# Performance work log

Measured on AMD Instinct MI355X. Metric: run time of the kernel, lower is better.

The kernel has to match this reference:

```python
import jax, jax.numpy as jnp
import numpy as np

B, P, D_IN, D_MOD, N_HEADS = 512, 64, 64, 256, 4

def _ln(x, g, b):
    m = x.mean(-1, keepdims=True)
    v = ((x - m) ** 2).mean(-1, keepdims=True)
    return (x - m) / jnp.sqrt(v + 1e-5) * g + b

def _lin(x, w, b):
    return x @ w.T + b

def _mha(q, k, v, in_w, in_b, out_w, out_b, n_heads):
    # Faithful to torch nn.MultiheadAttention(batch_first=False): dim0=seq, dim1=batch.
    S, N, E = q.shape
    dh = E // n_heads
    wq, wk, wv = jnp.split(in_w, 3, axis=0)
    bq, bk, bv = jnp.split(in_b, 3)
    qp = _lin(q, wq, bq).reshape(S, N, n_heads, dh)
    kp = _lin(k, wk, bk).reshape(S, N, n_heads, dh)
    vp = _lin(v, wv, bv).reshape(S, N, n_heads, dh)
    scores = jnp.einsum('snhd,tnhd->nhst', qp, kp) * (1.0 / np.sqrt(dh))
    attn = jax.nn.softmax(scores, axis=-1)
    o = jnp.einsum('nhst,tnhd->snhd', attn, vp).reshape(S, N, E)
    return _lin(o, out_w, out_b)

def _forward(x, emb_w, emb_b, emb_g, emb_beta, post_w, post_b, post_g, post_beta,
             attn_qw, attn_qb, attn_kw, attn_kb, attn_vw, attn_vb,
             attn_inw, attn_inb, attn_outw, attn_outb, attn_g, attn_beta,
             player_w, player_b, player_g, player_beta,
             team_w, team_b, team_g, team_beta,
             pre_w, pre_b, pre_g, pre_beta, lnf_g, lnf_b, pred_w, pred_b):
    # embedding: LinearWithLayerNorm = LayerNorm(Linear(x))
    p = _ln(_lin(x, emb_w, emb_b), emb_g, emb_beta)
    # post_embedding: ResidualLinearWithLayerNorm = LayerNorm(Linear(x)) + x
    p = _ln(_lin(p, post_w, post_b), post_g, post_beta) + p
    for i in range(2):
        res = p
        q = _lin(p, attn_qw[i], attn_qb[i])
        k = _lin(p, attn_kw[i], attn_kb[i])
        v = _lin(p, attn_vw[i], attn_vb[i])
        a = _mha(q, k, v, attn_inw[i], attn_inb[i], attn_outw[i], attn_outb[i], N_HEADS)
        p = _ln(a, attn_g[i], attn_beta[i]) + res
    for i in range(2):
        p = _ln(_lin(p, player_w[i], player_b[i]), player_g[i], player_beta[i]) + p
    # segment reduce: padded-ragged scatter + sum == masked sum over the player axis.
    # NOTE: original code computes BOTH masks as original[:,:,-1]==1 (bug preserved).
    mask = (x[:, :, -1] == 1).astype(p.dtype)  # [B, P]
    home = jnp.einsum('bpd,bp->bd', p, mask)
    away = home
    teams = jnp.concatenate([home, away], axis=1)  # [B, 2*d_mod]
    for i in range(2):
        teams = _ln(_lin(teams, team_w[i], team_b[i]), team_g[i], team_beta[i]) + teams
    o = _ln(_lin(teams, pre_w, pre_b), pre_g, pre_beta)
    o = _ln(o, lnf_g, lnf_b)
    o = _lin(o, pred_w, pred_b)[:, 0]  # squeeze(dim=1)
    return o


def setup_inputs() -> dict:
    key = jax.random.key(0)
    ks = iter(jax.random.split(key, 64))
    def nrm(shape):
        return jax.random.normal(next(ks), shape, jnp.float32) * 0.02
    x = jax.random.normal(next(ks), (B, P, D_IN), jnp.float32)
    flag = jax.random.bernoulli(next(ks), 0.5, (B, P)).astype(jnp.float32)
    x = x.at[:, :, -1].set(flag)  # binary home-team indicator channel
    d, d2 = D_MOD, 2 * D_MOD
    return dict(
        x=x,
        emb_w=nrm((d, D_IN)), emb_b=jnp.zeros(d), emb_g=jnp.ones(d), emb_beta=jnp.zeros(d),
        post_w=nrm((d, d)), post_b=jnp.zeros(d), post_g=jnp.ones(d), post_beta=jnp.zeros(d),
        attn_qw=nrm((2, d, d)), attn_qb=jnp.zeros((2, d)),
        attn_kw=nrm((2, d, d)), attn_kb=jnp.zeros((2, d)),
        attn_vw=nrm((2, d, d)), attn_vb=jnp.zeros((2, d)),
        attn_inw=nrm((2, 3 * d, d)), attn_inb=jnp.zeros((2, 3 * d)),
        attn_outw=nrm((2, d, d)), attn_outb=jnp.zeros((2, d)),
        attn_g=jnp.ones((2, d)), attn_beta=jnp.zeros((2, d)),
        player_w=nrm((2, d, d)), player_b=jnp.zeros((2, d)),
        player_g=jnp.ones((2, d)), player_beta=jnp.zeros((2, d)),
        team_w=nrm((2, d2, d2)), team_b=jnp.zeros((2, d2)),
        team_g=jnp.ones((2, d2)), team_beta=jnp.zeros((2, d2)),
        pre_w=nrm((d, d2)), pre_b=jnp.zeros(d), pre_g=jnp.ones(d), pre_beta=jnp.zeros(d),
        lnf_g=jnp.ones(d), lnf_b=jnp.zeros(d),
        pred_w=nrm((1, d)), pred_b=jnp.zeros(1),
    )


def reference(x, emb_w, emb_b, emb_g, emb_beta, post_w, post_b, post_g, post_beta,
              attn_qw, attn_qb, attn_kw, attn_kb, attn_vw, attn_vb,
              attn_inw, attn_inb, attn_outw, attn_outb, attn_g, attn_beta,
              player_w, player_b, player_g, player_beta,
              team_w, team_b, team_g, team_beta,
              pre_w, pre_b, pre_g, pre_beta, lnf_g, lnf_b, pred_w, pred_b):
    return _forward(x, emb_w, emb_b, emb_g, emb_beta, post_w, post_b, post_g, post_beta,
                    attn_qw, attn_qb, attn_kw, attn_kb, attn_vw, attn_vb,
                    attn_inw, attn_inb, attn_outw, attn_outb, attn_g, attn_beta,
                    player_w, player_b, player_g, player_beta,
                    team_w, team_b, team_g, team_beta,
                    pre_w, pre_b, pre_g, pre_beta, lnf_g, lnf_b, pred_w, pred_b)
```

## Files before the change

### kernel.cpp

```cpp
#include <hip/hip_runtime.h>
#include <math.h>


typedef __bf16 bf16x8 __attribute__((ext_vector_type(8)));
typedef __bf16 bf16x4 __attribute__((ext_vector_type(4)));
typedef __bf16 bf16x2 __attribute__((ext_vector_type(2)));
typedef float  f32x4  __attribute__((ext_vector_type(4)));
typedef unsigned short u16;
typedef unsigned short u16x8 __attribute__((ext_vector_type(8)));

__device__ __forceinline__ u16 f2b(float f) {
    unsigned int u = __builtin_bit_cast(unsigned int, f);
    return (u16)((u + 0x7fffu + ((u >> 16) & 1u)) >> 16);
}
__device__ __forceinline__ float b2f(u16 u) {
    unsigned int v = ((unsigned int)u) << 16;
    return __builtin_bit_cast(float, v);
}
__device__ __forceinline__ bf16x8 ld2x64(const u16* p) {
    bf16x4 lo = *(const bf16x4*)p;
    bf16x4 hi = *(const bf16x4*)(p + 4);
    return __builtin_shufflevector(lo, hi, 0, 1, 2, 3, 4, 5, 6, 7);
}
__device__ __forceinline__ bf16x8 ld4x32(const u16* p) {
    bf16x2 a = *(const bf16x2*)p,     b = *(const bf16x2*)(p + 2);
    bf16x2 c = *(const bf16x2*)(p + 4), d = *(const bf16x2*)(p + 6);
    bf16x4 lo = __builtin_shufflevector(a, b, 0, 1, 2, 3);
    bf16x4 hi = __builtin_shufflevector(c, d, 0, 1, 2, 3);
    return __builtin_shufflevector(lo, hi, 0, 1, 2, 3, 4, 5, 6, 7);
}
__device__ __forceinline__ void split8(const float* __restrict__ s,
                                       bf16x8& hi, bf16x8& lo) {
    u16x8 h, l;
    #pragma unroll
    for (int j = 0; j < 8; ++j) {
        float v  = s[j];
        u16  hb  = f2b(v);
        h[j] = hb;
        l[j] = f2b(v - b2f(hb));
    }
    hi = __builtin_bit_cast(bf16x8, h);
    lo = __builtin_bit_cast(bf16x8, l);
}

template<int IN, bool LN, bool RES, bool AF32, int OMODE, bool TEAM>
__device__ __forceinline__
void gemm_body(const void* __restrict__ Xa, const void* __restrict__ Xb, int ldX,
               const u16* __restrict__ Whi, const u16* __restrict__ Wlo,
               const float* __restrict__ bias,
               const float* __restrict__ g, const float* __restrict__ beta,
               const u16* __restrict__ resh, const u16* __restrict__ resl,
               int ldRes, void* __restrict__ Y0, void* __restrict__ Y1, int ldY,
               const float* __restrict__ xmask, float* __restrict__ teams,
               u16* __restrict__ Wb)
{
    constexpr int KT = IN / 32;
    const int tid = threadIdx.x;
    const int wv = tid >> 6, lane = tid & 63;
    const int quad = lane >> 4, l16 = lane & 15;
    const long arow = (long)blockIdx.x * 64 + wv * 16 + l16;

    const u16* sbase[8];
    int sdst[8];
    #pragma unroll
    for (int i = 0; i < 8; ++i) {
        int cid = tid + i * 256;
        int plane = cid >> 10, nt = (cid >> 6) & 15, slot = cid & 63;
        int q = slot >> 4, c = slot & 15;
        sbase[i] = (plane ? Wlo : Whi) + (long)(nt * 16 + c) * IN + q * 8;
        sdst[i]  = (plane * 16 + nt) * 512 + slot * 8;
    }
    u16x8 wreg[8];
    auto issueW = [&](int kt) {
        #pragma unroll
        for (int i = 0; i < 8; ++i) wreg[i] = *(const u16x8*)(sbase[i] + kt * 32);
    };
    auto commitW = [&](int buf) {
        #pragma unroll
        for (int i = 0; i < 8; ++i)
            *(u16x8*)&Wb[buf * 16384 + sdst[i]] = wreg[i];
    };

    bf16x8 ah[3], al[3];
    auto loadA = [&](int kt) {
        int s = kt % 3;
        long aofs = arow * (long)ldX + kt * 32 + quad * 8;
        if constexpr (AF32) {
            float av[8];
            *(f32x4*)&av[0] = *(const f32x4*)&((const float*)Xa)[aofs];
            *(f32x4*)&av[4] = *(const f32x4*)&((const float*)Xa)[aofs + 4];
            split8(av, ah[s], al[s]);
        } else {
            ah[s] = *(const bf16x8*)&((const u16*)Xa)[aofs];
            al[s] = *(const bf16x8*)&((const u16*)Xb)[aofs];
        }
    };

    f32x4 acc[16];
    #pragma unroll
    for (int nt = 0; nt < 16; ++nt) acc[nt] = f32x4{0.f, 0.f, 0.f, 0.f};

    issueW(0);
    commitW(0);
    if (KT > 1) issueW(1);
    loadA(0);
    if (KT > 1) loadA(1);
    __syncthreads();

    #pragma unroll
    for (int kt = 0; kt < KT; ++kt) {
        if (kt + 2 < KT) loadA(kt + 2);
        const u16* wb = Wb + (kt & 1) * 16384;
        const int s = kt % 3;
        #pragma unroll
        for (int nt = 0; nt < 16; ++nt) {
            bf16x8 bhi = *(const bf16x8*)&wb[nt * 512 + lane * 8];
            bf16x8 blo = *(const bf16x8*)&wb[(16 + nt) * 512 + lane * 8];
            acc[nt] = __builtin_amdgcn_mfma_f32_16x16x32_bf16(al[s], bhi, acc[nt], 0, 0, 0);
            acc[nt] = __builtin_amdgcn_mfma_f32_16x16x32_bf16(ah[s], blo, acc[nt], 0, 0, 0);
            acc[nt] = __builtin_amdgcn_mfma_f32_16x16x32_bf16(ah[s], bhi, acc[nt], 0, 0, 0);
        }
        if (kt + 1 < KT) {
            commitW((kt + 1) & 1);
            if (kt + 2 < KT) issueW(kt + 2);
            __syncthreads();
        }
    }

    #pragma unroll
    for (int nt = 0; nt < 16; ++nt) {
        float bc = bias[nt * 16 + l16];
        #pragma unroll
        for (int r = 0; r < 4; ++r) acc[nt][r] += bc;
    }

    float mean[4], rstd[4];
    if constexpr (LN) {
        float s1[4] = {0, 0, 0, 0}, s2[4] = {0, 0, 0, 0};
        #pragma unroll
        for (int nt = 0; nt < 16; ++nt)
            #pragma unroll
            for (int r = 0; r < 4; ++r) {
                s1[r] += acc[nt][r];
                s2[r] += acc[nt][r] * acc[nt][r];
            }
        #pragma unroll
        for (int off = 1; off < 16; off <<= 1)
            #pragma unroll
            for (int r = 0; r < 4; ++r) {
                s1[r] += __shfl_xor(s1[r], off, 64);
                s2[r] += __shfl_xor(s2[r], off, 64);
            }
        #pragma unroll
        for (int r = 0; r < 4; ++r) {
            mean[r] = s1[r] * (1.0f / 256.f);
            float var = s2[r] * (1.0f / 256.f) - mean[r] * mean[r];
            rstd[r] = rsqrtf(var + 1e-5f);
        }
    }

    if constexpr (TEAM) {
        float m[4];
        #pragma unroll
        for (int r = 0; r < 4; ++r) {
            long row = (long)blockIdx.x * 64 + wv * 16 + quad * 4 + r;
            m[r] = (xmask[row * 64 + 63] == 1.0f) ? 1.0f : 0.0f;
        }
        float ts[16];
        #pragma unroll
        for (int nt = 0; nt < 16; ++nt) {
            int col = nt * 16 + l16;
            float gc = g[col], bc2 = beta[col];
            ts[nt] = 0.f;
            #pragma unroll
            for (int r = 0; r < 4; ++r) {
                long row = (long)blockIdx.x * 64 + wv * 16 + quad * 4 + r;
                float v = (acc[nt][r] - mean[r]) * rstd[r] * gc + bc2;
                v += b2f(resh[row * ldRes + col]) + b2f(resl[row * ldRes + col]);
                ts[nt] += m[r] * v;
            }
        }
        #pragma unroll
        for (int nt = 0; nt < 16; ++nt) {
            ts[nt] += __shfl_xor(ts[nt], 16, 64);
            ts[nt] += __shfl_xor(ts[nt], 32, 64);
        }
        __syncthreads();
        float* tsum = (float*)Wb;
        if (quad == 0) {
            #pragma unroll
            for (int nt = 0; nt < 16; ++nt)
                tsum[wv * 256 + nt * 16 + l16] = ts[nt];
        }
        __syncthreads();
        if (tid < 256) {
            float tot = tsum[tid] + tsum[256 + tid]
                      + tsum[512 + tid] + tsum[768 + tid];
            teams[(long)blockIdx.x * 512 + tid]       = tot;
            teams[(long)blockIdx.x * 512 + 256 + tid] = tot;
        }
        return;
    }

    #pragma unroll
    for (int nt = 0; nt < 16; ++nt) {
        int col = nt * 16 + l16;
        float gc = 1.f, bc2 = 0.f;
        if constexpr (LN) { gc = g[col]; bc2 = beta[col]; }
        #pragma unroll
        for (int r = 0; r < 4; ++r) {
            long row = (long)blockIdx.x * 64 + wv * 16 + quad * 4 + r;
            float v = acc[nt][r];
            if constexpr (LN) v = (v - mean[r]) * rstd[r] * gc + bc2;
            if constexpr (RES)
                v += b2f(resh[row * ldRes + col]) + b2f(resl[row * ldRes + col]);
            long yofs = row * ldY + col;
            if constexpr (OMODE == 0) {
                ((float*)Y0)[yofs] = v;
            } else if constexpr (OMODE == 1) {
                u16 hb = f2b(v);
                ((u16*)Y0)[yofs] = hb;
                ((u16*)Y1)[yofs] = f2b(v - b2f(hb));
            } else if constexpr (OMODE == 2) {
                ((u16*)Y0)[yofs] = f2b(v);
            } else {
                long idx = ((long)((row & 63) * 4 + (col >> 6)) * 512
                            + (row >> 6)) * 64 + (col & 63);
                ((u16*)Y0)[idx] = f2b(v);
            }
        }
    }
}

template<int IN, bool LN, bool RES, bool AF32, int OMODE, bool TEAM>
__global__ __launch_bounds__(256)
void gemm_kernel(const void* __restrict__ Xa, const void* __restrict__ Xb, int ldX,
                 const u16* __restrict__ Whi, const u16* __restrict__ Wlo,
                 const float* __restrict__ bias,
                 const float* __restrict__ g, const float* __restrict__ beta,
                 const u16* __restrict__ resh, const u16* __restrict__ resl,
                 int ldRes, void* __restrict__ Y0, void* __restrict__ Y1, int ldY,
                 const float* __restrict__ xmask, float* __restrict__ teams)
{
    __shared__ u16 Wb[32768];
    gemm_body<IN, LN, RES, AF32, OMODE, TEAM>(Xa, Xb, ldX, Whi, Wlo, bias, g,
                                              beta, resh, resl, ldRes, Y0, Y1,
                                              ldY, xmask, teams, Wb);
}

__global__ __launch_bounds__(256)
void qkv_proj(const u16* __restrict__ ph, const u16* __restrict__ pl,
              const u16* __restrict__ cwL, const float* __restrict__ cb,
              u16* __restrict__ qb, u16* __restrict__ kb, u16* __restrict__ vh)
{
    __shared__ u16 Wb[32768];
    int wsel = blockIdx.y;
    const u16* whi = cwL + (long)wsel * 65536;
    const u16* wlo = cwL + 393216 + (long)wsel * 65536;
    u16* Y = (wsel == 0) ? qb : (wsel == 1) ? kb : vh;
    gemm_body<256, false, false, false, 3, false>(
        ph, pl, 256, whi, wlo, cb + wsel * 256, nullptr, nullptr,
        nullptr, nullptr, 0, Y, nullptr, 256, nullptr, nullptr, Wb);
}

__global__ __launch_bounds__(256)
void combine_kernel(const float* __restrict__ inw, const float* __restrict__ inb,
                    const float* __restrict__ qw, const float* __restrict__ kw,
                    const float* __restrict__ vw, const float* __restrict__ qb,
                    const float* __restrict__ kb, const float* __restrict__ vb,
                    u16* __restrict__ cw, float* __restrict__ cb)
{
    int idx = blockIdx.y, L = idx / 3, wsel = idx % 3;
    const float* Wa = inw + (long)L * 768 * 256 + wsel * 65536;
    const float* ba = inb + L * 768 + wsel * 256;
    const float* Wf = (wsel == 0 ? qw : wsel == 1 ? kw : vw) + (long)L * 65536;
    const float* bf = (wsel == 0 ? qb : wsel == 1 ? kb : vb) + L * 256;

    int o = blockIdx.x, j = threadIdx.x;
    float s = 0.f;
    for (int mm = 0; mm < 256; ++mm)
        s += Wa[o * 256 + mm] * Wf[mm * 256 + j];
    u16 hb = f2b(s);
    cw[(long)idx * 65536 + o * 256 + j] = hb;
    cw[393216 + (long)idx * 65536 + o * 256 + j] = f2b(s - b2f(hb));

    __shared__ float red[256];
    red[j] = Wa[o * 256 + j] * bf[j];
    __syncthreads();
    for (int st = 128; st > 0; st >>= 1) {
        if (j < st) red[j] += red[j + st];
        __syncthreads();
    }
    if (j == 0) cb[idx * 256 + o] = red[0] + ba[o];
}

__global__ __launch_bounds__(256)
void cast_split_multi(const float* s0, u16* d0, int n0,
                      const float* s1, u16* d1, int n1,
                      const float* s2, u16* d2, int n2,
                      const float* s3, u16* d3, int n3,
                      const float* s4, u16* d4, int n4,
                      const float* s5, u16* d5, int n5)
{
    const float* s; u16* d; int n;
    switch (blockIdx.y) {
        case 0: s = s0; d = d0; n = n0; break;
        case 1: s = s1; d = d1; n = n1; break;
        case 2: s = s2; d = d2; n = n2; break;
        case 3: s = s3; d = d3; n = n3; break;
        case 4: s = s4; d = d4; n = n4; break;
        default: s = s5; d = d5; n = n5; break;
    }
    int i = (blockIdx.x * 256 + threadIdx.x) * 4;
    if (i >= n) return;
    float4 v = *(const float4*)&s[i];
    ushort4 h, l;
    h.x = f2b(v.x); l.x = f2b(v.x - b2f(h.x));
    h.y = f2b(v.y); l.y = f2b(v.y - b2f(h.y));
    h.z = f2b(v.z); l.z = f2b(v.z - b2f(h.z));
    h.w = f2b(v.w); l.w = f2b(v.w - b2f(h.w));
    *(ushort4*)&d[i] = h;
    *(ushort4*)&d[n + i] = l;
}

#define VTS 66
#define PS  68
#define EXP2SCALE 0.18033688089184986f

__global__ __launch_bounds__(256)
void attn_kernel(const u16* __restrict__ qbuf, const u16* __restrict__ kbuf,
                 const u16* __restrict__ vh,
                 u16* __restrict__ ofh, u16* __restrict__ ofl)
{
    const int n = blockIdx.x, h = blockIdx.y, sq = blockIdx.z;
    const int tid = threadIdx.x;
    const int wv = tid >> 6, lane = tid & 63;
    const int quad = lane >> 4, l16 = lane & 15;
    const long nhb = (long)(n * 4 + h) * 32768;

    __shared__ u16 Vth[64 * VTS];
    __shared__ u16 Pbh[4][32 * PS];

    bf16x8 qf[2][2];
    #pragma unroll
    for (int rt = 0; rt < 2; ++rt)
        #pragma unroll
        for (int kc = 0; kc < 2; ++kc) {
            long s = sq * 128 + wv * 32 + rt * 16 + l16;
            qf[rt][kc] = *(const bf16x8*)&qbuf[nhb + s * 64 + kc * 32 + quad * 8];
        }

    f32x4 o[2][4];
    #pragma unroll
    for (int rt = 0; rt < 2; ++rt)
        #pragma unroll
        for (int dt = 0; dt < 4; ++dt) o[rt][dt] = f32x4{0.f, 0.f, 0.f, 0.f};
    float l_run[2][4] = {{0.f, 0.f, 0.f, 0.f}, {0.f, 0.f, 0.f, 0.f}};

    for (int tb = 0; tb < 8; ++tb) {
        __syncthreads();
        for (int i = tid; i < 512; i += 256) {
            int t = i >> 3, c = i & 7;
            u16x8 hvv = *(const u16x8*)&vh[nhb + (long)(tb * 64 + t) * 64 + c * 8];
            #pragma unroll
            for (int j = 0; j < 8; ++j)
                Vth[(c * 8 + j) * VTS + t] = hvv[j];
        }
        __syncthreads();

        f32x4 sA[2][4];
        #pragma unroll
        for (int rt = 0; rt < 2; ++rt)
            #pragma unroll
            for (int tt = 0; tt < 4; ++tt) sA[rt][tt] = f32x4{0.f, 0.f, 0.f, 0.f};
        #pragma unroll
        for (int kc = 0; kc < 2; ++kc)
            #pragma unroll
            for (int tt = 0; tt < 4; ++tt) {
                bf16x8 kf = *(const bf16x8*)
                    &kbuf[nhb + (long)(tb * 64 + tt * 16 + l16) * 64
                          + kc * 32 + quad * 8];
                sA[0][tt] = __builtin_amdgcn_mfma_f32_16x16x32_bf16(
                    qf[0][kc], kf, sA[0][tt], 0, 0, 0);
                sA[1][tt] = __builtin_amdgcn_mfma_f32_16x16x32_bf16(
                    qf[1][kc], kf, sA[1][tt], 0, 0, 0);
            }

        #pragma unroll
        for (int rt = 0; rt < 2; ++rt)
            #pragma unroll
            for (int r = 0; r < 4; ++r) {
                float p0 = exp2f(sA[rt][0][r] * EXP2SCALE);
                float p1 = exp2f(sA[rt][1][r] * EXP2SCALE);
                float p2 = exp2f(sA[rt][2][r] * EXP2SCALE);
                float p3 = exp2f(sA[rt][3][r] * EXP2SCALE);
                int prow = (rt * 16 + quad * 4 + r) * PS + l16;
                Pbh[wv][prow +  0] = f2b(p0);
                Pbh[wv][prow + 16] = f2b(p1);
                Pbh[wv][prow + 32] = f2b(p2);
                Pbh[wv][prow + 48] = f2b(p3);
                l_run[rt][r] += (p0 + p1) + (p2 + p3);
            }

        #pragma unroll
        for (int kc = 0; kc < 2; ++kc) {
            bf16x8 pfh[2];
            #pragma unroll
            for (int rt = 0; rt < 2; ++rt)
                pfh[rt] = ld2x64(&Pbh[wv][(rt * 16 + l16) * PS
                                          + kc * 32 + quad * 8]);
            #pragma unroll
            for (int dt = 0; dt < 4; ++dt) {
                bf16x8 vfh = ld4x32(&Vth[(dt * 16 + l16) * VTS
                                         + kc * 32 + quad * 8]);
                o[0][dt] = __builtin_amdgcn_mfma_f32_16x16x32_bf16(
                    pfh[0], vfh, o[0][dt], 0, 0, 0);
                o[1][dt] = __builtin_amdgcn_mfma_f32_16x16x32_bf16(
                    pfh[1], vfh, o[1][dt], 0, 0, 0);
            }
        }
    }

    #pragma unroll
    for (int off = 1; off < 16; off <<= 1)
        #pragma unroll
        for (int rt = 0; rt < 2; ++rt)
            #pragma unroll
            for (int r = 0; r < 4; ++r)
                l_run[rt][r] += __shfl_xor(l_run[rt][r], off, 64);

    #pragma unroll
    for (int rt = 0; rt < 2; ++rt)
        #pragma unroll
        for (int r = 0; r < 4; ++r) {
            float inv = 1.0f / l_run[rt][r];
            long s = sq * 128 + wv * 32 + rt * 16 + quad * 4 + r;
            #pragma unroll
            for (int dt = 0; dt < 4; ++dt) {
                long idx = (s * 64 + n) * 256 + h * 64 + dt * 16 + l16;
                float val = o[rt][dt][r] * inv;
                u16 hb = f2b(val);
                ofh[idx] = hb;
                ofl[idx] = f2b(val - b2f(hb));
            }
        }
}

template<int IN, int OUT, bool RES>
__global__ __launch_bounds__(256)
void tail_gemm(const float* __restrict__ X,
               const u16* __restrict__ Whi, const u16* __restrict__ Wlo,
               const float* __restrict__ bias,
               const float* __restrict__ g, const float* __restrict__ beta,
               const float* __restrict__ res, float* __restrict__ Y)
{
    constexpr int NTW = OUT / 64;
    constexpr int KT  = IN / 32;
    const int tid = threadIdx.x;
    const int wv = tid >> 6, lane = tid & 63;
    const int quad = lane >> 4, l16 = lane & 15;
    const int row0 = blockIdx.x * 16;
    const int colbase = wv * (OUT / 4);

    f32x4 acc[NTW];
    #pragma unroll
    for (int nt = 0; nt < NTW; ++nt) acc[nt] = f32x4{0.f, 0.f, 0.f, 0.f};

    #pragma unroll
    for (int kt = 0; kt < KT; ++kt) {
        float av[8];
        long aofs = (long)(row0 + l16) * IN + kt * 32 + quad * 8;
        *(f32x4*)&av[0] = *(const f32x4*)&X[aofs];
        *(f32x4*)&av[4] = *(const f32x4*)&X[aofs + 4];
        bf16x8 ah, al;
        split8(av, ah, al);
        #pragma unroll
        for (int nt = 0; nt < NTW; ++nt) {
            long wofs = (long)(colbase + nt * 16 + l16) * IN + kt * 32 + quad * 8;
            bf16x8 bhi = *(const bf16x8*)&Whi[wofs];
            bf16x8 blo = *(const bf16x8*)&Wlo[wofs];
            acc[nt] = __builtin_amdgcn_mfma_f32_16x16x32_bf16(al, bhi, acc[nt], 0, 0, 0);
            acc[nt] = __builtin_amdgcn_mfma_f32_16x16x32_bf16(ah, blo, acc[nt], 0, 0, 0);
            acc[nt] = __builtin_amdgcn_mfma_f32_16x16x32_bf16(ah, bhi, acc[nt], 0, 0, 0);
        }
    }

    #pragma unroll
    for (int nt = 0; nt < NTW; ++nt) {
        float bc = bias[colbase + nt * 16 + l16];
        #pragma unroll
        for (int r = 0; r < 4; ++r) acc[nt][r] += bc;
    }

    float s1[4] = {0, 0, 0, 0}, s2[4] = {0, 0, 0, 0};
    #pragma unroll
    for (int nt = 0; nt < NTW; ++nt)
        #pragma unroll
        for (int r = 0; r < 4; ++r) {
            s1[r] += acc[nt][r];
            s2[r] += acc[nt][r] * acc[nt][r];
        }
    #pragma unroll
    for (int off = 1; off < 16; off <<= 1)
        #pragma unroll
        for (int r = 0; r < 4; ++r) {
            s1[r] += __shfl_xor(s1[r], off, 64);
            s2[r] += __shfl_xor(s2[r], off, 64);
        }
    __shared__ float r1[64], r2[64];
    if (l16 == 0) {
        #pragma unroll
        for (int r = 0; r < 4; ++r) {
            r1[wv * 16 + quad * 4 + r] = s1[r];
            r2[wv * 16 + quad * 4 + r] = s2[r];
        }
    }
    __syncthreads();
    float mean[4], rstd[4];
    #pragma unroll
    for (int r = 0; r < 4; ++r) {
        int rr = quad * 4 + r;
        float t1 = r1[rr] + r1[16 + rr] + r1[32 + rr] + r1[48 + rr];
        float t2 = r2[rr] + r2[16 + rr] + r2[32 + rr] + r2[48 + rr];
        mean[r] = t1 * (1.0f / OUT);
        float var = t2 * (1.0f / OUT) - mean[r] * mean[r];
        rstd[r] = rsqrtf(var + 1e-5f);
    }
    #pragma unroll
    for (int nt = 0; nt < NTW; ++nt) {
        int col = colbase + nt * 16 + l16;
        float gc = g[col], bc2 = beta[col];
        #pragma unroll
        for (int r = 0; r < 4; ++r) {
            int row = row0 + quad * 4 + r;
            float v = (acc[nt][r] - mean[r]) * rstd[r] * gc + bc2;
            if constexpr (RES) v += res[(long)row * OUT + col];
            Y[(long)row * OUT + col] = v;
        }
    }
}

__global__ __launch_bounds__(256)
void tail_pred(const float* __restrict__ X,
               const u16* __restrict__ Whi, const u16* __restrict__ Wlo,
               const float* __restrict__ bias,
               const float* __restrict__ g, const float* __restrict__ beta,
               const float* __restrict__ lnf_g, const float* __restrict__ lnf_b,
               const float* __restrict__ pw, const float* __restrict__ pb,
               float* __restrict__ out)
{
    constexpr int IN = 512, OUT = 256, NTW = 4, KT = 16;
    const int tid = threadIdx.x;
    const int wv = tid >> 6, lane = tid & 63;
    const int quad = lane >> 4, l16 = lane & 15;
    const int row0 = blockIdx.x * 16;
    const int colbase = wv * 64;

    f32x4 acc[NTW];
    #pragma unroll
    for (int nt = 0; nt < NTW; ++nt) acc[nt] = f32x4{0.f, 0.f, 0.f, 0.f};

    #pragma unroll
    for (int kt = 0; kt < KT; ++kt) {
        float av[8];
        long aofs = (long)(row0 + l16) * IN + kt * 32 + quad * 8;
        *(f32x4*)&av[0] = *(const f32x4*)&X[aofs];
        *(f32x4*)&av[4] = *(const f32x4*)&X[aofs + 4];
        bf16x8 ah, al;
        split8(av, ah, al);
        #pragma unroll
        for (int nt = 0; nt < NTW; ++nt) {
            long wofs = (long)(colbase + nt * 16 + l16) * IN + kt * 32 + quad * 8;
            bf16x8 bhi = *(const bf16x8*)&Whi[wofs];
            bf16x8 blo = *(const bf16x8*)&Wlo[wofs];
            acc[nt] = __builtin_amdgcn_mfma_f32_16x16x32_bf16(al, bhi, acc[nt], 0, 0, 0);
            acc[nt] = __builtin_amdgcn_mfma_f32_16x16x32_bf16(ah, blo, acc[nt], 0, 0, 0);
            acc[nt] = __builtin_amdgcn_mfma_f32_16x16x32_bf16(ah, bhi, acc[nt], 0, 0, 0);
        }
    }
    #pragma unroll
    for (int nt = 0; nt < NTW; ++nt) {
        float bc = bias[colbase + nt * 16 + l16];
        #pragma unroll
        for (int r = 0; r < 4; ++r) acc[nt][r] += bc;
    }

    __shared__ float r1[64], r2[64];
    float s1[4] = {0, 0, 0, 0}, s2[4] = {0, 0, 0, 0};
    #pragma unroll
    for (int nt = 0; nt < NTW; ++nt)
        #pragma unroll
        for (int r = 0; r < 4; ++r) {
            s1[r] += acc[nt][r];
            s2[r] += acc[nt][r] * acc[nt][r];
        }
    #pragma unroll
    for (int off = 1; off < 16; off <<= 1)
        #pragma unroll
        for (int r = 0; r < 4; ++r) {
            s1[r] += __shfl_xor(s1[r], off, 64);
            s2[r] += __shfl_xor(s2[r], off, 64);
        }
    if (l16 == 0)
        #pragma unroll
        for (int r = 0; r < 4; ++r) {
            r1[wv * 16 + quad * 4 + r] = s1[r];
            r2[wv * 16 + quad * 4 + r] = s2[r];
        }
    __syncthreads();
    float vv[NTW][4];
    #pragma unroll
    for (int r = 0; r < 4; ++r) {
        int rr = quad * 4 + r;
        float t1 = r1[rr] + r1[16 + rr] + r1[32 + rr] + r1[48 + rr];
        float t2 = r2[rr] + r2[16 + rr] + r2[32 + rr] + r2[48 + rr];
        float mean = t1 * (1.0f / OUT);
        float rstd = rsqrtf(t2 * (1.0f / OUT) - mean * mean + 1e-5f);
        #pragma unroll
        for (int nt = 0; nt < NTW; ++nt) {
            int col = colbase + nt * 16 + l16;
            vv[nt][r] = (acc[nt][r] - mean) * rstd * g[col] + beta[col];
        }
    }
    float u1[4] = {0, 0, 0, 0}, u2[4] = {0, 0, 0, 0};
    #pragma unroll
    for (int nt = 0; nt < NTW; ++nt)
        #pragma unroll
        for (int r = 0; r < 4; ++r) {
            u1[r] += vv[nt][r];
            u2[r] += vv[nt][r] * vv[nt][r];
        }
    #pragma unroll
    for (int off = 1; off < 16; off <<= 1)
        #pragma unroll
        for (int r = 0; r < 4; ++r) {
            u1[r] += __shfl_xor(u1[r], off, 64);
            u2[r] += __shfl_xor(u2[r], off, 64);
        }
    __syncthreads();
    if (l16 == 0)
        #pragma unroll
        for (int r = 0; r < 4; ++r) {
            r1[wv * 16 + quad * 4 + r] = u1[r];
            r2[wv * 16 + quad * 4 + r] = u2[r];
        }
    __syncthreads();
    float pd[4];
    #pragma unroll
    for (int r = 0; r < 4; ++r) {
        int rr = quad * 4 + r;
        float t1 = r1[rr] + r1[16 + rr] + r1[32 + rr] + r1[48 + rr];
        float t2 = r2[rr] + r2[16 + rr] + r2[32 + rr] + r2[48 + rr];
        float mean = t1 * (1.0f / OUT);
        float rstd = rsqrtf(t2 * (1.0f / OUT) - mean * mean + 1e-5f);
        pd[r] = 0.f;
        #pragma unroll
        for (int nt = 0; nt < NTW; ++nt) {
            int col = colbase + nt * 16 + l16;
            float v2 = (vv[nt][r] - mean) * rstd * lnf_g[col] + lnf_b[col];
            pd[r] += v2 * pw[col];
        }
    }
    #pragma unroll
    for (int off = 1; off < 16; off <<= 1)
        #pragma unroll
        for (int r = 0; r < 4; ++r)
            pd[r] += __shfl_xor(pd[r], off, 64);
    __syncthreads();
    if (l16 == 0)
        #pragma unroll
        for (int r = 0; r < 4; ++r)
            r1[wv * 16 + quad * 4 + r] = pd[r];
    __syncthreads();
    if (wv == 0 && l16 == 0) {
        #pragma unroll
        for (int r = 0; r < 4; ++r) {
            int rr = quad * 4 + r;
            out[row0 + rr] = r1[rr] + r1[16 + rr] + r1[32 + rr] + r1[48 + rr]
                           + pb[0];
        }
    }
}

extern "C" void kernel_launch(void* const* d_in, const int* in_sizes, int n_in,
                              void* d_out, int out_size, void* d_ws, size_t ws_size,
                              hipStream_t stream)
{
    const float* x         = (const float*)d_in[0];
    const float* emb_w     = (const float*)d_in[1];
    const float* emb_b     = (const float*)d_in[2];
    const float* emb_g     = (const float*)d_in[3];
    const float* emb_beta  = (const float*)d_in[4];
    const float* post_w    = (const float*)d_in[5];
    const float* post_b    = (const float*)d_in[6];
    const float* post_g    = (const float*)d_in[7];
    const float* post_beta = (const float*)d_in[8];
    const float* attn_qw   = (const float*)d_in[9];
    const float* attn_qb   = (const float*)d_in[10];
    const float* attn_kw   = (const float*)d_in[11];
    const float* attn_kb   = (const float*)d_in[12];
    const float* attn_vw   = (const float*)d_in[13];
    const float* attn_vb   = (const float*)d_in[14];
    const float* attn_inw  = (const float*)d_in[15];
    const float* attn_inb  = (const float*)d_in[16];
    const float* attn_outw = (const float*)d_in[17];
    const float* attn_outb = (const float*)d_in[18];
    const float* attn_g    = (const float*)d_in[19];
    const float* attn_beta = (const float*)d_in[20];
    const float* player_w  = (const float*)d_in[21];
    const float* player_b  = (const float*)d_in[22];
    const float* player_g  = (const float*)d_in[23];
    const float* player_bt = (const float*)d_in[24];
    const float* team_w    = (const float*)d_in[25];
    const float* team_b    = (const float*)d_in[26];
    const float* team_g    = (const float*)d_in[27];
    const float* team_beta = (const float*)d_in[28];
    const float* pre_w     = (const float*)d_in[29];
    const float* pre_b     = (const float*)d_in[30];
    const float* pre_g     = (const float*)d_in[31];
    const float* pre_beta  = (const float*)d_in[32];
    const float* lnf_g     = (const float*)d_in[33];
    const float* lnf_b     = (const float*)d_in[34];
    const float* pred_w    = (const float*)d_in[35];
    const float* pred_b    = (const float*)d_in[36];

    char* base = (char*)d_ws;
    const size_t NR = (size_t)32768 * 256;
    u16* ph  = (u16*)base;  base += NR * 2;
    u16* pl  = (u16*)base;  base += NR * 2;
    u16* ofh = (u16*)base;  base += NR * 2;
    u16* ofl = (u16*)base;  base += NR * 2;
    u16* vh  = (u16*)base;  base += NR * 2;
    u16* qb  = (u16*)base;  base += NR * 2;
    u16* kb  = (u16*)base;  base += NR * 2;
    float* teams0 = (float*)base; base += (size_t)512 * 512 * 4;
    float* teams1 = (float*)base; base += (size_t)512 * 512 * 4;
    u16* emb_wp    = (u16*)base;  base += (size_t)2 * 16384 * 2;
    u16* post_wp   = (u16*)base;  base += (size_t)2 * 65536 * 2;
    u16* outw_p    = (u16*)base;  base += (size_t)2 * 131072 * 2;
    u16* player_wp = (u16*)base;  base += (size_t)2 * 131072 * 2;
    u16* team_wp   = (u16*)base;  base += (size_t)2 * 524288 * 2;
    u16* pre_wp    = (u16*)base;  base += (size_t)2 * 131072 * 2;
    u16* cwb       = (u16*)base;  base += (size_t)2 * 393216 * 2;
    float* cbf     = (float*)base; base += (size_t)1536 * 4;

    cast_split_multi<<<dim3(512, 6), 256, 0, stream>>>(
        emb_w, emb_wp, 16384,
        post_w, post_wp, 65536,
        attn_outw, outw_p, 131072,
        player_w, player_wp, 131072,
        team_w, team_wp, 524288,
        pre_w, pre_wp, 131072);

    combine_kernel<<<dim3(256, 6), 256, 0, stream>>>(
        attn_inw, attn_inb, attn_qw, attn_kw, attn_vw,
        attn_qb, attn_kb, attn_vb, cwb, cbf);

    gemm_kernel<64, true, false, true, 1, false><<<512, 256, 0, stream>>>(
        x, nullptr, 64, emb_wp, emb_wp + 16384, emb_b, emb_g, emb_beta,
        nullptr, nullptr, 0, ph, pl, 256, nullptr, nullptr);
    gemm_kernel<256, true, true, false, 1, false><<<512, 256, 0, stream>>>(
        ph, pl, 256, post_wp, post_wp + 65536, post_b, post_g, post_beta,
        ph, pl, 256, ph, pl, 256, nullptr, nullptr);

    for (int L = 0; L < 2; ++L) {
        qkv_proj<<<dim3(512, 3), 256, 0, stream>>>(
            ph, pl, cwb + (size_t)L * 3 * 65536, cbf + L * 768, qb, kb, vh);
        attn_kernel<<<dim3(64, 4, 4), 256, 0, stream>>>(qb, kb, vh, ofh, ofl);
        gemm_kernel<256, true, true, false, 1, false><<<512, 256, 0, stream>>>(
            ofh, ofl, 256, outw_p + (size_t)L * 65536,
            outw_p + 131072 + (size_t)L * 65536, attn_outb + L * 256,
            attn_g + L * 256, attn_beta + L * 256, ph, pl, 256, ph, pl, 256,
            nullptr, nullptr);
    }

    gemm_kernel<256, true, true, false, 1, false><<<512, 256, 0, stream>>>(
        ph, pl, 256, player_wp, player_wp + 131072, player_b,
        player_g, player_bt, ph, pl, 256, ph, pl, 256, nullptr, nullptr);
    gemm_kernel<256, true, true, false, 1, true><<<512, 256, 0, stream>>>(
        ph, pl, 256, player_wp + 65536, player_wp + 131072 + 65536,
        player_b + 256, player_g + 256, player_bt + 256, ph, pl, 256,
        nullptr, nullptr, 256, x, teams0);

    tail_gemm<512, 512, true><<<32, 256, 0, stream>>>(
        teams0, team_wp, team_wp + 524288, team_b,
        team_g, team_beta, teams0, teams1);
    tail_gemm<512, 512, true><<<32, 256, 0, stream>>>(
        teams1, team_wp + 262144, team_wp + 524288 + 262144, team_b + 512,
        team_g + 512, team_beta + 512, teams1, teams0);

    tail_pred<<<32, 256, 0, stream>>>(
        teams0, pre_wp, pre_wp + 131072, pre_b, pre_g, pre_beta,
        lnf_g, lnf_b, pred_w, pred_b, (float*)d_out);
}
```

Baseline: 745.4 us.

## Double-buffer V tile and prefetch K/V into registers in attention kernel

Replaces the two-barrier synchronous V load per key block with a double-buffered LDS tile: V for block tb+2 is prefetched into registers and committed to the alternate buffer while block tb is computed. K fragments for the next block are also prefetched into registers after the QK MFMAs, so global latency overlaps the softmax and PV work. The loop is fully unrolled, there is one barrier per iteration, and the launch bound now requests 4 blocks per CU. This raises register and LDS use, which could cost occupancy or cause spills. It only speeds up the attention part of the larger forward pass.

```diff
diff --git a/kernel.cpp b/kernel.cpp
--- a/kernel.cpp
+++ b/kernel.cpp
@@ -327,7 +327,7 @@
 #define PS  68
 #define EXP2SCALE 0.18033688089184986f
 
-__global__ __launch_bounds__(256)
+__global__ __launch_bounds__(256, 4)
 void attn_kernel(const u16* __restrict__ qbuf, const u16* __restrict__ kbuf,
                  const u16* __restrict__ vh,
                  u16* __restrict__ ofh, u16* __restrict__ ofl)
@@ -338,7 +338,7 @@
     const int quad = lane >> 4, l16 = lane & 15;
     const long nhb = (long)(n * 4 + h) * 32768;
 
-    __shared__ u16 Vth[64 * VTS];
+    __shared__ u16 Vth[2][64 * VTS];
     __shared__ u16 Pbh[4][32 * PS];
 
     bf16x8 qf[2][2];
@@ -350,6 +350,34 @@
             qf[rt][kc] = *(const bf16x8*)&qbuf[nhb + s * 64 + kc * 32 + quad * 8];
         }
 
+    const int vt = tid >> 3, vc = tid & 7;
+    const int vt2 = (tid + 256) >> 3, vc2 = (tid + 256) & 7;
+
+    u16x8 vreg[2];
+    auto loadV = [&](int tb) {
+        vreg[0] = *(const u16x8*)&vh[nhb + (long)(tb * 64 + vt) * 64 + vc * 8];
+        vreg[1] = *(const u16x8*)&vh[nhb + (long)(tb * 64 + vt2) * 64 + vc2 * 8];
+    };
+    auto commitV = [&](int buf) {
+        #pragma unroll
+        for (int j = 0; j < 8; ++j)
+            Vth[buf][(vc * 8 + j) * VTS + vt] = vreg[0][j];
+        #pragma unroll
+        for (int j = 0; j < 8; ++j)
+            Vth[buf][(vc2 * 8 + j) * VTS + vt2] = vreg[1][j];
+    };
+
+    bf16x8 kreg[2][4];
+    auto loadK = [&](int tb) {
+        #pragma unroll
+        for (int kc = 0; kc < 2; ++kc)
+            #pragma unroll
+            for (int tt = 0; tt < 4; ++tt)
+                kreg[kc][tt] = *(const bf16x8*)
+                    &kbuf[nhb + (long)(tb * 64 + tt * 16 + l16) * 64
+                          + kc * 32 + quad * 8];
+    };
+
     f32x4 o[2][4];
     #pragma unroll
     for (int rt = 0; rt < 2; ++rt)
@@ -357,16 +385,15 @@
         for (int dt = 0; dt < 4; ++dt) o[rt][dt] = f32x4{0.f, 0.f, 0.f, 0.f};
     float l_run[2][4] = {{0.f, 0.f, 0.f, 0.f}, {0.f, 0.f, 0.f, 0.f}};
 
+    loadV(0);
+    loadK(0);
+    commitV(0);
+    loadV(1);
+    __syncthreads();
+
+    #pragma unroll
     for (int tb = 0; tb < 8; ++tb) {
-        __syncthreads();
-        for (int i = tid; i < 512; i += 256) {
-            int t = i >> 3, c = i & 7;
-            u16x8 hvv = *(const u16x8*)&vh[nhb + (long)(tb * 64 + t) * 64 + c * 8];
-            #pragma unroll
-            for (int j = 0; j < 8; ++j)
-                Vth[(c * 8 + j) * VTS + t] = hvv[j];
-        }
-        __syncthreads();
+        if (tb + 1 < 8) commitV((tb + 1) & 1);
 
         f32x4 sA[2][4];
         #pragma unroll
@@ -377,14 +404,14 @@
         for (int kc = 0; kc < 2; ++kc)
             #pragma unroll
             for (int tt = 0; tt < 4; ++tt) {
-                bf16x8 kf = *(const bf16x8*)
-                    &kbuf[nhb + (long)(tb * 64 + tt * 16 + l16) * 64
-                          + kc * 32 + quad * 8];
                 sA[0][tt] = __builtin_amdgcn_mfma_f32_16x16x32_bf16(
-                    qf[0][kc], kf, sA[0][tt], 0, 0, 0);
+                    qf[0][kc], kreg[kc][tt], sA[0][tt], 0, 0, 0);
                 sA[1][tt] = __builtin_amdgcn_mfma_f32_16x16x32_bf16(
-                    qf[1][kc], kf, sA[1][tt], 0, 0, 0);
+                    qf[1][kc], kreg[kc][tt], sA[1][tt], 0, 0, 0);
             }
+
+        if (tb + 1 < 8) loadK(tb + 1);
+        if (tb + 2 < 8) loadV(tb + 2);
 
         #pragma unroll
         for (int rt = 0; rt < 2; ++rt)
@@ -411,14 +438,16 @@
                                           + kc * 32 + quad * 8]);
             #pragma unroll
             for (int dt = 0; dt < 4; ++dt) {
-                bf16x8 vfh = ld4x32(&Vth[(dt * 16 + l16) * VTS
-                                         + kc * 32 + quad * 8]);
+                bf16x8 vfh = ld4x32(&Vth[tb & 1][(dt * 16 + l16) * VTS
+                                                 + kc * 32 + quad * 8]);
                 o[0][dt] = __builtin_amdgcn_mfma_f32_16x16x32_bf16(
                     pfh[0], vfh, o[0][dt], 0, 0, 0);
                 o[1][dt] = __builtin_amdgcn_mfma_f32_16x16x32_bf16(
                     pfh[1], vfh, o[1][dt], 0, 0, 0);
             }
         }
+
+        __syncthreads();
     }
 
     #pragma unroll
```

Measured after the change: 1.026 ms. +37.7%, slower.

## Split attention key range across waves and reduce partial outputs in shared memory

Applied to the files above, without the earlier changes.

The attention kernel now gives each block 32 query rows, and each of its four waves handles a disjoint quarter of the keys (two 64-key tiles) with a private V-transpose and P buffer. This removes the per-tile block-wide barriers and grows the grid fourfold. After the loop the waves write their partial outputs and row sums to shared memory, then sum them cooperatively. This is valid because no running max is used. The cost is a larger shared-memory footprint (50KB per block), which may limit occupancy, plus an extra reduction pass. Q fragments are now loaded redundantly by all four waves.

```diff
diff --git a/kernel.cpp b/kernel.cpp
--- a/kernel.cpp
+++ b/kernel.cpp
@@ -338,15 +338,17 @@
     const int quad = lane >> 4, l16 = lane & 15;
     const long nhb = (long)(n * 4 + h) * 32768;
 
-    __shared__ u16 Vth[64 * VTS];
-    __shared__ u16 Pbh[4][32 * PS];
+    __shared__ __align__(16) char smem[51200];
+    u16* SM = (u16*)smem;
+    u16* Vw = SM + wv * (64 * VTS);
+    u16* Pw = SM + 4 * (64 * VTS) + wv * (32 * PS);
 
     bf16x8 qf[2][2];
     #pragma unroll
     for (int rt = 0; rt < 2; ++rt)
         #pragma unroll
         for (int kc = 0; kc < 2; ++kc) {
-            long s = sq * 128 + wv * 32 + rt * 16 + l16;
+            long s = sq * 32 + rt * 16 + l16;
             qf[rt][kc] = *(const bf16x8*)&qbuf[nhb + s * 64 + kc * 32 + quad * 8];
         }
 
@@ -357,16 +359,19 @@
         for (int dt = 0; dt < 4; ++dt) o[rt][dt] = f32x4{0.f, 0.f, 0.f, 0.f};
     float l_run[2][4] = {{0.f, 0.f, 0.f, 0.f}, {0.f, 0.f, 0.f, 0.f}};
 
-    for (int tb = 0; tb < 8; ++tb) {
-        __syncthreads();
-        for (int i = tid; i < 512; i += 256) {
-            int t = i >> 3, c = i & 7;
+    #pragma unroll
+    for (int ti = 0; ti < 2; ++ti) {
+        const int tb = wv * 2 + ti;
+
+        #pragma unroll
+        for (int i = 0; i < 8; ++i) {
+            int idx = lane + i * 64;
+            int t = idx >> 3, c = idx & 7;
             u16x8 hvv = *(const u16x8*)&vh[nhb + (long)(tb * 64 + t) * 64 + c * 8];
             #pragma unroll
             for (int j = 0; j < 8; ++j)
-                Vth[(c * 8 + j) * VTS + t] = hvv[j];
-        }
-        __syncthreads();
+                Vw[(c * 8 + j) * VTS + t] = hvv[j];
+        }
 
         f32x4 sA[2][4];
         #pragma unroll
@@ -395,10 +400,10 @@
                 float p2 = exp2f(sA[rt][2][r] * EXP2SCALE);
                 float p3 = exp2f(sA[rt][3][r] * EXP2SCALE);
                 int prow = (rt * 16 + quad * 4 + r) * PS + l16;
-                Pbh[wv][prow +  0] = f2b(p0);
-                Pbh[wv][prow + 16] = f2b(p1);
-                Pbh[wv][prow + 32] = f2b(p2);
-                Pbh[wv][prow + 48] = f2b(p3);
+                Pw[prow +  0] = f2b(p0);
+                Pw[prow + 16] = f2b(p1);
+                Pw[prow + 32] = f2b(p2);
+                Pw[prow + 48] = f2b(p3);
                 l_run[rt][r] += (p0 + p1) + (p2 + p3);
             }
 
@@ -407,12 +412,11 @@
             bf16x8 pfh[2];
             #pragma unroll
             for (int rt = 0; rt < 2; ++rt)
-                pfh[rt] = ld2x64(&Pbh[wv][(rt * 16 + l16) * PS
-                                          + kc * 32 + quad * 8]);
+                pfh[rt] = ld2x64(&Pw[(rt * 16 + l16) * PS + kc * 32 + quad * 8]);
             #pragma unroll
             for (int dt = 0; dt < 4; ++dt) {
-                bf16x8 vfh = ld4x32(&Vth[(dt * 16 + l16) * VTS
-                                         + kc * 32 + quad * 8]);
+                bf16x8 vfh = ld4x32(&Vw[(dt * 16 + l16) * VTS
+                                        + kc * 32 + quad * 8]);
                 o[0][dt] = __builtin_amdgcn_mfma_f32_16x16x32_bf16(
                     pfh[0], vfh, o[0][dt], 0, 0, 0);
                 o[1][dt] = __builtin_amdgcn_mfma_f32_16x16x32_bf16(
@@ -421,28 +425,61 @@
         }
     }
 
+    __syncthreads();
+    float* os = (float*)smem;
+    float* ls = (float*)(smem + 36864);
+    {
+        int base = (wv * 64 + lane) * 36;
+        #pragma unroll
+        for (int rt = 0; rt < 2; ++rt)
+            #pragma unroll
+            for (int dt = 0; dt < 4; ++dt)
+                *(f32x4*)&os[base + (rt * 4 + dt) * 4] = o[rt][dt];
+        int lbase = (wv * 64 + lane) * 9;
+        #pragma unroll
+        for (int rt = 0; rt < 2; ++rt)
+            #pragma unroll
+            for (int r = 0; r < 4; ++r)
+                ls[lbase + rt * 4 + r] = l_run[rt][r];
+    }
+    __syncthreads();
+
+    f32x4 osum[2];
+    float lsum[2][4];
+    #pragma unroll
+    for (int rt = 0; rt < 2; ++rt) {
+        osum[rt] = f32x4{0.f, 0.f, 0.f, 0.f};
+        #pragma unroll
+        for (int w = 0; w < 4; ++w)
+            osum[rt] += *(const f32x4*)&os[(w * 64 + lane) * 36 + (rt * 4 + wv) * 4];
+        #pragma unroll
+        for (int r = 0; r < 4; ++r) {
+            float acc = 0.f;
+            #pragma unroll
+            for (int w = 0; w < 4; ++w)
+                acc += ls[(w * 64 + lane) * 9 + rt * 4 + r];
+            lsum[rt][r] = acc;
+        }
+    }
     #pragma unroll
     for (int off = 1; off < 16; off <<= 1)
         #pragma unroll
         for (int rt = 0; rt < 2; ++rt)
             #pragma unroll
             for (int r = 0; r < 4; ++r)
-                l_run[rt][r] += __shfl_xor(l_run[rt][r], off, 64);
+                lsum[rt][r] += __shfl_xor(lsum[rt][r], off, 64);
 
     #pragma unroll
     for (int rt = 0; rt < 2; ++rt)
         #pragma unroll
         for (int r = 0; r < 4; ++r) {
-            float inv = 1.0f / l_run[rt][r];
-            long s = sq * 128 + wv * 32 + rt * 16 + quad * 4 + r;
-            #pragma unroll
-            for (int dt = 0; dt < 4; ++dt) {
-                long idx = (s * 64 + n) * 256 + h * 64 + dt * 16 + l16;
-                float val = o[rt][dt][r] * inv;
-                u16 hb = f2b(val);
-                ofh[idx] = hb;
-                ofl[idx] = f2b(val - b2f(hb));
-            }
+            float inv = 1.0f / lsum[rt][r];
+            long s = sq * 32 + rt * 16 + quad * 4 + r;
+            long idx = (s * 64 + n) * 256 + h * 64 + wv * 16 + l16;
+            float val = osum[rt][r] * inv;
+            u16 hb = f2b(val);
+            ofh[idx] = hb;
+            ofl[idx] = f2b(val - b2f(hb));
         }
 }
 
@@ -766,7 +803,7 @@
     for (int L = 0; L < 2; ++L) {
         qkv_proj<<<dim3(512, 3), 256, 0, stream>>>(
             ph, pl, cwb + (size_t)L * 3 * 65536, cbf + L * 768, qb, kb, vh);
-        attn_kernel<<<dim3(64, 4, 4), 256, 0, stream>>>(qb, kb, vh, ofh, ofl);
+        attn_kernel<<<dim3(64, 4, 16), 256, 0, stream>>>(qb, kb, vh, ofh, ofl);
         gemm_kernel<256, true, true, false, 1, false><<<512, 256, 0, stream>>>(
             ofh, ofl, 256, outw_p + (size_t)L * 65536,
             outw_p + 131072 + (size_t)L * 65536, attn_outb + L * 256,
```

Result: slower. 767.5 us (+3.0%).

## Pre-transpose V in a separate kernel and read it directly in attention

Applied to the files above, without the earlier changes.

Adds a vtrans_kernel that writes V per (batch, head) in a transposed [d][t] layout to a new workspace buffer. The attention kernel then loads V fragments for the PV MFMA straight from global memory as 16-byte vectors. This removes the per-tile LDS transpose and its two __syncthreads from the attention loop. The cost is an extra kernel launch per layer plus a full extra write and read of V, and the four sq-blocks that share a head each re-read V from global or L2 instead of sharing it through LDS.

```diff
diff --git a/kernel.cpp b/kernel.cpp
--- a/kernel.cpp
+++ b/kernel.cpp
@@ -20,13 +20,6 @@
 __device__ __forceinline__ bf16x8 ld2x64(const u16* p) {
     bf16x4 lo = *(const bf16x4*)p;
     bf16x4 hi = *(const bf16x4*)(p + 4);
-    return __builtin_shufflevector(lo, hi, 0, 1, 2, 3, 4, 5, 6, 7);
-}
-__device__ __forceinline__ bf16x8 ld4x32(const u16* p) {
-    bf16x2 a = *(const bf16x2*)p,     b = *(const bf16x2*)(p + 2);
-    bf16x2 c = *(const bf16x2*)(p + 4), d = *(const bf16x2*)(p + 6);
-    bf16x4 lo = __builtin_shufflevector(a, b, 0, 1, 2, 3);
-    bf16x4 hi = __builtin_shufflevector(c, d, 0, 1, 2, 3);
     return __builtin_shufflevector(lo, hi, 0, 1, 2, 3, 4, 5, 6, 7);
 }
 __device__ __forceinline__ void split8(const float* __restrict__ s,
@@ -323,13 +316,37 @@
     *(ushort4*)&d[n + i] = l;
 }
 
-#define VTS 66
+#define TPD 66
+__global__ __launch_bounds__(256)
+void vtrans_kernel(const u16* __restrict__ vh, u16* __restrict__ vt)
+{
+    const long nhb = (long)blockIdx.x * 32768;
+    const int tid = threadIdx.x;
+    const int rs = tid >> 2, cc = tid & 3;
+    __shared__ u16 T[64 * TPD];
+    for (int st = 0; st < 8; ++st) {
+        if (st) __syncthreads();
+        *(u16x8*)&T[rs * TPD + cc * 16] =
+            *(const u16x8*)&vh[nhb + (long)(st * 64 + rs) * 64 + cc * 16];
+        *(u16x8*)&T[rs * TPD + cc * 16 + 8] =
+            *(const u16x8*)&vh[nhb + (long)(st * 64 + rs) * 64 + cc * 16 + 8];
+        __syncthreads();
+        u16x8 a, b;
+        #pragma unroll
+        for (int m = 0; m < 8; ++m) a[m] = T[(cc * 16 + m) * TPD + rs];
+        #pragma unroll
+        for (int m = 0; m < 8; ++m) b[m] = T[(cc * 16 + 8 + m) * TPD + rs];
+        *(u16x8*)&vt[nhb + (long)rs * 512 + st * 64 + cc * 16]     = a;
+        *(u16x8*)&vt[nhb + (long)rs * 512 + st * 64 + cc * 16 + 8] = b;
+    }
+}
+
 #define PS  68
 #define EXP2SCALE 0.18033688089184986f
 
 __global__ __launch_bounds__(256)
 void attn_kernel(const u16* __restrict__ qbuf, const u16* __restrict__ kbuf,
-                 const u16* __restrict__ vh,
+                 const u16* __restrict__ vt,
                  u16* __restrict__ ofh, u16* __restrict__ ofl)
 {
     const int n = blockIdx.x, h = blockIdx.y, sq = blockIdx.z;
@@ -338,8 +355,8 @@
     const int quad = lane >> 4, l16 = lane & 15;
     const long nhb = (long)(n * 4 + h) * 32768;
 
-    __shared__ u16 Vth[64 * VTS];
     __shared__ u16 Pbh[4][32 * PS];
+    u16* Pw = Pbh[wv];
 
     bf16x8 qf[2][2];
     #pragma unroll
@@ -357,17 +374,8 @@
         for (int dt = 0; dt < 4; ++dt) o[rt][dt] = f32x4{0.f, 0.f, 0.f, 0.f};
     float l_run[2][4] = {{0.f, 0.f, 0.f, 0.f}, {0.f, 0.f, 0.f, 0.f}};
 
+    #pragma unroll 1
     for (int tb = 0; tb < 8; ++tb) {
-        __syncthreads();
-        for (int i = tid; i < 512; i += 256) {
-            int t = i >> 3, c = i & 7;
-            u16x8 hvv = *(const u16x8*)&vh[nhb + (long)(tb * 64 + t) * 64 + c * 8];
-            #pragma unroll
-            for (int j = 0; j < 8; ++j)
-                Vth[(c * 8 + j) * VTS + t] = hvv[j];
-        }
-        __syncthreads();
-
         f32x4 sA[2][4];
         #pragma unroll
         for (int rt = 0; rt < 2; ++rt)
@@ -395,10 +403,10 @@
                 float p2 = exp2f(sA[rt][2][r] * EXP2SCALE);
                 float p3 = exp2f(sA[rt][3][r] * EXP2SCALE);
                 int prow = (rt * 16 + quad * 4 + r) * PS + l16;
-                Pbh[wv][prow +  0] = f2b(p0);
-                Pbh[wv][prow + 16] = f2b(p1);
-                Pbh[wv][prow + 32] = f2b(p2);
-                Pbh[wv][prow + 48] = f2b(p3);
+                Pw[prow +  0] = f2b(p0);
+                Pw[prow + 16] = f2b(p1);
+                Pw[prow + 32] = f2b(p2);
+                Pw[prow + 48] = f2b(p3);
                 l_run[rt][r] += (p0 + p1) + (p2 + p3);
             }
 
@@ -407,16 +415,16 @@
             bf16x8 pfh[2];
             #pragma unroll
             for (int rt = 0; rt < 2; ++rt)
-                pfh[rt] = ld2x64(&Pbh[wv][(rt * 16 + l16) * PS
-                                          + kc * 32 + quad * 8]);
+                pfh[rt] = ld2x64(&Pw[(rt * 16 + l16) * PS + kc * 32 + quad * 8]);
             #pragma unroll
             for (int dt = 0; dt < 4; ++dt) {
-                bf16x8 vfh = ld4x32(&Vth[(dt * 16 + l16) * VTS
-                                         + kc * 32 + quad * 8]);
+                bf16x8 vf = *(const bf16x8*)
+                    &vt[nhb + (long)(dt * 16 + l16) * 512 + tb * 64
+                        + kc * 32 + quad * 8];
                 o[0][dt] = __builtin_amdgcn_mfma_f32_16x16x32_bf16(
-                    pfh[0], vfh, o[0][dt], 0, 0, 0);
+                    pfh[0], vf, o[0][dt], 0, 0, 0);
                 o[1][dt] = __builtin_amdgcn_mfma_f32_16x16x32_bf16(
-                    pfh[1], vfh, o[1][dt], 0, 0, 0);
+                    pfh[1], vf, o[1][dt], 0, 0, 0);
             }
         }
     }
@@ -733,6 +741,7 @@
     u16* vh  = (u16*)base;  base += NR * 2;
     u16* qb  = (u16*)base;  base += NR * 2;
     u16* kb  = (u16*)base;  base += NR * 2;
+    u16* vt  = (u16*)base;  base += NR * 2;
     float* teams0 = (float*)base; base += (size_t)512 * 512 * 4;
     float* teams1 = (float*)base; base += (size_t)512 * 512 * 4;
     u16* emb_wp    = (u16*)base;  base += (size_t)2 * 16384 * 2;
@@ -766,7 +775,8 @@
     for (int L = 0; L < 2; ++L) {
         qkv_proj<<<dim3(512, 3), 256, 0, stream>>>(
             ph, pl, cwb + (size_t)L * 3 * 65536, cbf + L * 768, qb, kb, vh);
-        attn_kernel<<<dim3(64, 4, 4), 256, 0, stream>>>(qb, kb, vh, ofh, ofl);
+        vtrans_kernel<<<256, 256, 0, stream>>>(vh, vt);
+        attn_kernel<<<dim3(64, 4, 4), 256, 0, stream>>>(qb, kb, vt, ofh, ofl);
         gemm_kernel<256, true, true, false, 1, false><<<512, 256, 0, stream>>>(
             ofh, ofl, 256, outw_p + (size_t)L * 65536,
             outw_p + 131072 + (size_t)L * 65536, attn_outb + L * 256,
```

Result: slower. 784.2 us (+5.2%).
